# Optimization experiments

Hardware: AMD Instinct MI355X
Metric: run time of the kernel (lower is better)

## Reference

```python
import jax, jax.numpy as jnp
import numpy as np

N_NODES = 100000
N_EDGES = 3200000
IN_DIM = 256
HID = 64
OUT_DIM = 1


def gcn_conv(x, W, b, src, dst, n):
    # PyG GCNConv: h = x @ W; add self loops; sym-normalize; aggregate; + b
    h = x @ W  # [N, F]
    # degrees include self loops (edge_weight = 1), computed on target nodes
    ones = jnp.ones(src.shape[0], dtype=x.dtype)
    deg = jax.ops.segment_sum(ones, dst, num_segments=n) + 1.0  # +1 for self loop
    dinv = jax.lax.rsqrt(deg)
    norm = dinv[src] * dinv[dst]  # [E]
    msg = h[src] * norm[:, None]  # gather + scale
    out = jax.ops.segment_sum(msg, dst, num_segments=n)
    # self-loop contribution: norm_ii = dinv[i]^2
    out = out + h * (dinv * dinv)[:, None]
    return out + b


def setup_inputs() -> dict:
    key = jax.random.key(0)
    ks = jax.random.split(key, 6)
    x = jax.random.normal(ks[0], (N_NODES, IN_DIM), dtype=jnp.float32)
    edge_index = jax.random.randint(ks[1], (2, N_EDGES), 0, N_NODES, dtype=jnp.int64)
    W1 = jax.random.normal(ks[2], (IN_DIM, HID), dtype=jnp.float32) / np.sqrt(IN_DIM)
    b1 = jnp.zeros((HID,), dtype=jnp.float32)
    W2 = jax.random.normal(ks[3], (HID, HID), dtype=jnp.float32) / np.sqrt(HID)
    b2 = jnp.zeros((HID,), dtype=jnp.float32)
    Wf = jax.random.normal(ks[4], (HID, OUT_DIM), dtype=jnp.float32) / np.sqrt(HID)
    bf = jnp.zeros((OUT_DIM,), dtype=jnp.float32)
    return {"x": x, "edge_index": edge_index, "W1": W1, "b1": b1,
            "W2": W2, "b2": b2, "Wf": Wf, "bf": bf}


def reference(x, edge_index, W1, b1, W2, b2, Wf, bf):
    src, dst = edge_index[0], edge_index[1]
    n = x.shape[0]
    h = jax.nn.relu(gcn_conv(x, W1, b1, src, dst, n))
    h = jax.nn.relu(gcn_conv(h, W2, b2, src, dst, n))
    g = jnp.mean(h, axis=0)  # [HID] graph readout
    return jax.nn.sigmoid(g @ Wf + bf)  # [OUT_DIM]
```

## Files before the change

### kernel.cpp

```cpp
#include <hip/hip_runtime.h>


typedef unsigned int u32;
typedef unsigned short u16;
typedef unsigned char u8;
typedef short s16x8 __attribute__((ext_vector_type(8)));
typedef __bf16 bf16x8 __attribute__((ext_vector_type(8)));
typedef float f32x4 __attribute__((ext_vector_type(4)));

constexpr int HID  = 64;
constexpr int SH   = 7;
constexpr int BK   = 128;
constexpr int BPAD = 1024;
constexpr int CH   = 4096;
constexpr int SLOT = 5120;
constexpr int NBLK2 = 4096;

static __device__ __forceinline__ u8 f2fp8(float f) {
    int p = __builtin_amdgcn_cvt_pk_fp8_f32(f, f, 0, false);
    return (u8)(p & 0xFF);
}
static __device__ __forceinline__ float fp82f(u8 v) {
    return __builtin_amdgcn_cvt_f32_fp8((int)v, 0);
}
static __device__ __forceinline__ u16 f2bf(float f) {
    u32 u = __float_as_uint(f);
    return (u16)((u + 0x7FFFu + ((u >> 16) & 1u)) >> 16);
}

__global__ void pack_both_kernel(const float* __restrict__ W1, const float* __restrict__ W2,
                                 u16* __restrict__ wpack1, u16* __restrict__ wpack2) {
    int i = blockIdx.x * 256 + threadIdx.x;
    if (i < 256 * 64) {
        int e = i & 7, lane = (i >> 3) & 63, nt = (i >> 9) & 3, kk = i >> 11;
        wpack1[i] = f2bf(W1[(kk * 32 + (lane >> 4) * 8 + e) * HID + nt * 16 + (lane & 15)]);
    } else {
        int j = i - 256 * 64;
        if (j < 64 * 64) {
            int e = j & 7, lane = (j >> 3) & 63, nt = (j >> 9) & 3, kk = j >> 11;
            wpack2[j] = f2bf(W2[(kk * 32 + (lane >> 4) * 8 + e) * HID + nt * 16 + (lane & 15)]);
        }
    }
}

__global__ __launch_bounds__(256) void mega1_kernel(const int* __restrict__ src,
                                                    const int* __restrict__ dst,
                                                    int* __restrict__ bcur,
                                                    u32* __restrict__ ep, int ne,
                                                    const float* __restrict__ x,
                                                    const u16* __restrict__ wpack1,
                                                    u8* __restrict__ hp, int n,
                                                    int PBLK, int GBLK) {
    __shared__ int hcnt[BPAD];
    __shared__ int hoff[BPAD];
    __shared__ int gbase[BPAD];
    __shared__ u32 stage[CH];
    __shared__ int ssc[256];
    const int t = threadIdx.x;

    if ((int)blockIdx.x < PBLK) {
        const int base = blockIdx.x * CH;
        const int cnt = min(CH, ne - base);
        for (int i = t; i < BPAD; i += 256) hcnt[i] = 0;
        __syncthreads();
        int myr[CH / 256];
        #pragma unroll
        for (int k = 0; k < CH / 256; ++k) {
            int i = t + k * 256;
            if (i < cnt) myr[k] = atomicAdd(&hcnt[dst[base + i] >> SH], 1);
        }
        __syncthreads();
        {
            int c0 = hcnt[t*4], c1 = hcnt[t*4+1], c2 = hcnt[t*4+2], c3 = hcnt[t*4+3];
            int tsum = c0 + c1 + c2 + c3;
            ssc[t] = tsum; __syncthreads();
            int run = tsum;
            for (int off = 1; off < 256; off <<= 1) {
                int v = (t >= off) ? ssc[t - off] : 0;
                __syncthreads();
                run += v; ssc[t] = run;
                __syncthreads();
            }
            int ex = run - tsum;
            hoff[t*4] = ex; ex += c0;
            hoff[t*4+1] = ex; ex += c1;
            hoff[t*4+2] = ex; ex += c2;
            hoff[t*4+3] = ex;
        }
        __syncthreads();
        for (int b = t; b < BPAD; b += 256) {
            int c = hcnt[b];
            if (c) gbase[b] = b * SLOT + atomicAdd(&bcur[b], c);
        }
        #pragma unroll
        for (int k = 0; k < CH / 256; ++k) {
            int i = t + k * 256;
            if (i < cnt) {
                int s = src[base + i], d = dst[base + i];
                stage[hoff[d >> SH] + myr[k]] = ((u32)(d & (BK - 1)) << 20) | (u32)s;
            }
        }
        __syncthreads();
        for (int i = t; i < cnt; i += 256) {
            u32 v = stage[i];
            int lo = 0;
            #pragma unroll
            for (int s = 512; s; s >>= 1) {
                int m = lo + s;
                if (m < BPAD && hoff[m] <= i) lo = m;
            }
            ep[gbase[lo] + (i - hoff[lo])] = v;
        }
    } else {
        const int gbid = blockIdx.x - PBLK;
        const int lane = t & 63;
        const int wid = t >> 6;
        const int r16 = lane & 15;
        const int kgrp = lane >> 4;
        const int ntiles = (n + 15) >> 4;
        for (int tile = gbid * 4 + wid; tile < ntiles; tile += GBLK * 4) {
            const int row0 = tile * 16;
            const int arow = row0 + r16;
            f32x4 acc[4] = {f32x4{0,0,0,0}, f32x4{0,0,0,0}, f32x4{0,0,0,0}, f32x4{0,0,0,0}};
            #pragma unroll
            for (int kk = 0; kk < 256 / 32; ++kk) {
                s16x8 abits;
                if (arow < n) {
                    const float4* p0 = (const float4*)(x + (size_t)arow * 256 + kk * 32 + kgrp * 8);
                    float4 v0 = p0[0], v1 = p0[1];
                    abits[0] = (short)f2bf(v0.x); abits[1] = (short)f2bf(v0.y);
                    abits[2] = (short)f2bf(v0.z); abits[3] = (short)f2bf(v0.w);
                    abits[4] = (short)f2bf(v1.x); abits[5] = (short)f2bf(v1.y);
                    abits[6] = (short)f2bf(v1.z); abits[7] = (short)f2bf(v1.w);
                } else {
                    #pragma unroll
                    for (int j = 0; j < 8; ++j) abits[j] = 0;
                }
                bf16x8 afrag = __builtin_bit_cast(bf16x8, abits);
                const u16* wp = wpack1 + ((size_t)(kk * 4) * 64 + lane) * 8;
                #pragma unroll
                for (int nt = 0; nt < 4; ++nt) {
                    bf16x8 bfrag = *(const bf16x8*)(wp + (size_t)nt * 64 * 8);
                    acc[nt] = __builtin_amdgcn_mfma_f32_16x16x32_bf16(afrag, bfrag, acc[nt], 0, 0, 0);
                }
            }
            #pragma unroll
            for (int reg = 0; reg < 4; ++reg) {
                int r = row0 + kgrp * 4 + reg;
                if (r < n) {
                    #pragma unroll
                    for (int nt = 0; nt < 4; ++nt)
                        hp[(size_t)r * HID + nt * 16 + r16] = f2fp8(acc[nt][reg]);
                }
            }
        }
    }
}

__global__ __launch_bounds__(256) void bucket_sort_kernel(const u32* __restrict__ ep,
                                                          const int* __restrict__ bcur,
                                                          int* __restrict__ eidx,
                                                          int* __restrict__ rowend,
                                                          float* __restrict__ dinv,
                                                          u8* __restrict__ hp, int n) {
    __shared__ int cnt[BK];
    __shared__ int sc[BK];
    __shared__ int cur[BK];
    __shared__ float sdv[BK];
    const int t = threadIdx.x, b = blockIdx.x;
    const int beg = b * SLOT, end = b * SLOT + bcur[b];
    if (t < BK) cnt[t] = 0;
    __syncthreads();
    for (int p = beg + t; p < end; p += 256) atomicAdd(&cnt[ep[p] >> 20], 1);
    __syncthreads();
    if (t < BK) sc[t] = cnt[t];
    __syncthreads();
    for (int o = 1; o < BK; o <<= 1) {
        int v = 0;
        if (t < BK && t >= o) v = sc[t - o];
        __syncthreads();
        if (t < BK) sc[t] += v;
        __syncthreads();
    }
    if (t < BK) {
        int node = b * BK + t;
        float dv = rsqrtf((float)cnt[t] + 1.0f);
        sdv[t] = dv;
        if (node < n) {
            rowend[node] = beg + sc[t];
            dinv[node] = dv;
        }
        cur[t] = beg + sc[t] - cnt[t];
    }
    __syncthreads();
    for (int p = beg + t; p < end; p += 256) {
        u32 v = ep[p];
        int r = atomicAdd(&cur[v >> 20], 1);
        eidx[r] = (int)(v & 0xFFFFFu);
    }
    u32* hp32 = (u32*)hp;
    const int base_node = b * BK;
    for (int i = t; i < BK * 16; i += 256) {
        int r = i >> 4;
        int node = base_node + r;
        if (node < n) {
            size_t off = (size_t)node * 16 + (i & 15);
            u32 v = hp32[off];
            float dv = sdv[r];
            float f0 = __builtin_amdgcn_cvt_f32_fp8((int)v, 0) * dv;
            float f1 = __builtin_amdgcn_cvt_f32_fp8((int)v, 1) * dv;
            float f2 = __builtin_amdgcn_cvt_f32_fp8((int)v, 2) * dv;
            float f3 = __builtin_amdgcn_cvt_f32_fp8((int)v, 3) * dv;
            int pk = __builtin_amdgcn_cvt_pk_fp8_f32(f0, f1, 0, false);
            pk = __builtin_amdgcn_cvt_pk_fp8_f32(f2, f3, pk, true);
            hp32[off] = (u32)pk;
        }
    }
}

__global__ __launch_bounds__(256) void mfma_gemm2_kernel(const u8* __restrict__ A,
                                                         const u16* __restrict__ wpack,
                                                         const float* __restrict__ dinv,
                                                         u8* __restrict__ out8, int n) {
    const int t = threadIdx.x;
    const int lane = t & 63;
    const int wid = t >> 6;
    const int r16 = lane & 15;
    const int kgrp = lane >> 4;
    const int ntiles = (n + 15) >> 4;
    for (int tile = blockIdx.x * 4 + wid; tile < ntiles; tile += gridDim.x * 4) {
        const int row0 = tile * 16;
        const int arow = row0 + r16;
        f32x4 acc[4] = {f32x4{0,0,0,0}, f32x4{0,0,0,0}, f32x4{0,0,0,0}, f32x4{0,0,0,0}};
        #pragma unroll
        for (int kk = 0; kk < 2; ++kk) {
            s16x8 abits;
            u32 w0 = 0, w1 = 0;
            if (arow < n) {
                const u32* p0 = (const u32*)(A + (size_t)arow * 64 + kk * 32 + kgrp * 8);
                w0 = p0[0]; w1 = p0[1];
            }
            abits[0] = (short)f2bf(__builtin_amdgcn_cvt_f32_fp8((int)w0, 0));
            abits[1] = (short)f2bf(__builtin_amdgcn_cvt_f32_fp8((int)w0, 1));
            abits[2] = (short)f2bf(__builtin_amdgcn_cvt_f32_fp8((int)w0, 2));
            abits[3] = (short)f2bf(__builtin_amdgcn_cvt_f32_fp8((int)w0, 3));
            abits[4] = (short)f2bf(__builtin_amdgcn_cvt_f32_fp8((int)w1, 0));
            abits[5] = (short)f2bf(__builtin_amdgcn_cvt_f32_fp8((int)w1, 1));
            abits[6] = (short)f2bf(__builtin_amdgcn_cvt_f32_fp8((int)w1, 2));
            abits[7] = (short)f2bf(__builtin_amdgcn_cvt_f32_fp8((int)w1, 3));
            bf16x8 afrag = __builtin_bit_cast(bf16x8, abits);
            const u16* wp = wpack + ((size_t)(kk * 4) * 64 + lane) * 8;
            #pragma unroll
            for (int nt = 0; nt < 4; ++nt) {
                bf16x8 bfrag = *(const bf16x8*)(wp + (size_t)nt * 64 * 8);
                acc[nt] = __builtin_amdgcn_mfma_f32_16x16x32_bf16(afrag, bfrag, acc[nt], 0, 0, 0);
            }
        }
        #pragma unroll
        for (int reg = 0; reg < 4; ++reg) {
            int r = row0 + kgrp * 4 + reg;
            if (r < n) {
                float dv = dinv[r];
                #pragma unroll
                for (int nt = 0; nt < 4; ++nt)
                    out8[(size_t)r * HID + nt * 16 + r16] = f2fp8(acc[nt][reg] * dv);
            }
        }
    }
}

#define CVT4(acc0, acc1, acc2, acc3, wv) \
    acc0 += __builtin_amdgcn_cvt_f32_fp8((int)(wv), 0); \
    acc1 += __builtin_amdgcn_cvt_f32_fp8((int)(wv), 1); \
    acc2 += __builtin_amdgcn_cvt_f32_fp8((int)(wv), 2); \
    acc3 += __builtin_amdgcn_cvt_f32_fp8((int)(wv), 3);

__global__ __launch_bounds__(256) void agg_csr_kernel(const u8* __restrict__ hp,
                                                      const int* __restrict__ eidx,
                                                      const int* __restrict__ rowend,
                                                      const float* __restrict__ dinv,
                                                      const float* __restrict__ bias,
                                                      u8* __restrict__ out, int n) {
    int w = (blockIdx.x * 256 + threadIdx.x) >> 6;
    int lane = threadIdx.x & 63;
    if (w >= n) return;
    const int g = lane >> 4, fb = lane & 15;
    int beg = (w & (BK - 1)) ? rowend[w - 1] : (w >> SH) * SLOT;
    int end = rowend[w];
    float a0 = 0.f, a1 = 0.f, a2 = 0.f, a3 = 0.f;
    int p = beg;
    for (; p + 16 <= end; p += 16) {
        int s0 = __builtin_nontemporal_load(eidx + p + g);
        int s1 = __builtin_nontemporal_load(eidx + p + 4 + g);
        int s2 = __builtin_nontemporal_load(eidx + p + 8 + g);
        int s3 = __builtin_nontemporal_load(eidx + p + 12 + g);
        u32 w0 = *(const u32*)(hp + (size_t)s0 * 64 + fb * 4);
        u32 w1 = *(const u32*)(hp + (size_t)s1 * 64 + fb * 4);
        u32 w2 = *(const u32*)(hp + (size_t)s2 * 64 + fb * 4);
        u32 w3 = *(const u32*)(hp + (size_t)s3 * 64 + fb * 4);
        CVT4(a0, a1, a2, a3, w0)
        CVT4(a0, a1, a2, a3, w1)
        CVT4(a0, a1, a2, a3, w2)
        CVT4(a0, a1, a2, a3, w3)
    }
    for (; p < end; p += 4) {
        int idx = p + g;
        bool valid = idx < end;
        int s = __builtin_nontemporal_load(eidx + (valid ? idx : beg));
        u32 wv = *(const u32*)(hp + (size_t)s * 64 + fb * 4);
        if (valid) { CVT4(a0, a1, a2, a3, wv) }
    }
    a0 += __shfl_xor(a0, 16); a0 += __shfl_xor(a0, 32);
    a1 += __shfl_xor(a1, 16); a1 += __shfl_xor(a1, 32);
    a2 += __shfl_xor(a2, 16); a2 += __shfl_xor(a2, 32);
    a3 += __shfl_xor(a3, 16); a3 += __shfl_xor(a3, 32);
    u32 sv = *(const u32*)(hp + (size_t)w * 64 + fb * 4);
    float dv = dinv[w];
    float v0 = fmaxf(dv * (a0 + __builtin_amdgcn_cvt_f32_fp8((int)sv, 0)) + bias[fb * 4 + 0], 0.f);
    float v1 = fmaxf(dv * (a1 + __builtin_amdgcn_cvt_f32_fp8((int)sv, 1)) + bias[fb * 4 + 1], 0.f);
    float v2 = fmaxf(dv * (a2 + __builtin_amdgcn_cvt_f32_fp8((int)sv, 2)) + bias[fb * 4 + 2], 0.f);
    float v3 = fmaxf(dv * (a3 + __builtin_amdgcn_cvt_f32_fp8((int)sv, 3)) + bias[fb * 4 + 3], 0.f);
    if (g == 0) {
        int r = __builtin_amdgcn_cvt_pk_fp8_f32(v0, v1, 0, false);
        r = __builtin_amdgcn_cvt_pk_fp8_f32(v2, v3, r, true);
        *(u32*)(out + (size_t)w * 64 + fb * 4) = (u32)r;
    }
}

__global__ __launch_bounds__(256) void agg_csr_reduce_kernel(const u8* __restrict__ hp,
                                                             const int* __restrict__ eidx,
                                                             const int* __restrict__ rowend,
                                                             const float* __restrict__ dinv,
                                                             const float* __restrict__ bias,
                                                             float* __restrict__ partials, int n) {
    __shared__ float sred[256];
    int t = threadIdx.x, lane = t & 63;
    const int g = lane >> 4, fb = lane & 15;
    int wid = (blockIdx.x * 256 + t) >> 6;
    int wstride = gridDim.x * 4;
    float bl0 = bias[fb * 4 + 0], bl1 = bias[fb * 4 + 1];
    float bl2 = bias[fb * 4 + 2], bl3 = bias[fb * 4 + 3];
    float t0 = 0.f, t1 = 0.f, t2 = 0.f, t3 = 0.f;
    for (int w = wid; w < n; w += wstride) {
        int beg = (w & (BK - 1)) ? rowend[w - 1] : (w >> SH) * SLOT;
        int end = rowend[w];
        float a0 = 0.f, a1 = 0.f, a2 = 0.f, a3 = 0.f;
        int p = beg;
        for (; p + 16 <= end; p += 16) {
            int s0 = __builtin_nontemporal_load(eidx + p + g);
            int s1 = __builtin_nontemporal_load(eidx + p + 4 + g);
            int s2 = __builtin_nontemporal_load(eidx + p + 8 + g);
            int s3 = __builtin_nontemporal_load(eidx + p + 12 + g);
            u32 w0 = *(const u32*)(hp + (size_t)s0 * 64 + fb * 4);
            u32 w1 = *(const u32*)(hp + (size_t)s1 * 64 + fb * 4);
            u32 w2 = *(const u32*)(hp + (size_t)s2 * 64 + fb * 4);
            u32 w3 = *(const u32*)(hp + (size_t)s3 * 64 + fb * 4);
            CVT4(a0, a1, a2, a3, w0)
            CVT4(a0, a1, a2, a3, w1)
            CVT4(a0, a1, a2, a3, w2)
            CVT4(a0, a1, a2, a3, w3)
        }
        for (; p < end; p += 4) {
            int idx = p + g;
            bool valid = idx < end;
            int s = __builtin_nontemporal_load(eidx + (valid ? idx : beg));
            u32 wv = *(const u32*)(hp + (size_t)s * 64 + fb * 4);
            if (valid) { CVT4(a0, a1, a2, a3, wv) }
        }
        a0 += __shfl_xor(a0, 16); a0 += __shfl_xor(a0, 32);
        a1 += __shfl_xor(a1, 16); a1 += __shfl_xor(a1, 32);
        a2 += __shfl_xor(a2, 16); a2 += __shfl_xor(a2, 32);
        a3 += __shfl_xor(a3, 16); a3 += __shfl_xor(a3, 32);
        u32 sv = *(const u32*)(hp + (size_t)w * 64 + fb * 4);
        float dv = dinv[w];
        t0 += fmaxf(dv * (a0 + __builtin_amdgcn_cvt_f32_fp8((int)sv, 0)) + bl0, 0.f);
        t1 += fmaxf(dv * (a1 + __builtin_amdgcn_cvt_f32_fp8((int)sv, 1)) + bl1, 0.f);
        t2 += fmaxf(dv * (a2 + __builtin_amdgcn_cvt_f32_fp8((int)sv, 2)) + bl2, 0.f);
        t3 += fmaxf(dv * (a3 + __builtin_amdgcn_cvt_f32_fp8((int)sv, 3)) + bl3, 0.f);
    }
    int wv_ = t >> 6;
    if (g == 0) {
        sred[wv_ * 64 + fb * 4 + 0] = t0;
        sred[wv_ * 64 + fb * 4 + 1] = t1;
        sred[wv_ * 64 + fb * 4 + 2] = t2;
        sred[wv_ * 64 + fb * 4 + 3] = t3;
    }
    __syncthreads();
    if (t < 64) partials[blockIdx.x * 64 + t] = sred[t] + sred[t + 64] + sred[t + 128] + sred[t + 192];
}

__global__ __launch_bounds__(256) void gsum_stage_kernel(const float* __restrict__ parts, int nblk,
                                                         float* __restrict__ gsum) {
    __shared__ float sred[256];
    int t = threadIdx.x, col = t & 63;
    float a = 0.f;
    for (int bk = blockIdx.x * 4 + (t >> 6); bk < nblk; bk += gridDim.x * 4)
        a += parts[bk * 64 + col];
    sred[t] = a; __syncthreads();
    if (t < 64) atomicAdd(&gsum[t], sred[t] + sred[t + 64] + sred[t + 128] + sred[t + 192]);
}

__global__ void final_gsum_kernel(const float* __restrict__ gsum, const float* __restrict__ Wf,
                                  const float* __restrict__ bf_, float* __restrict__ out, float invn) {
    int lane = threadIdx.x;
    float v = gsum[lane] * invn * Wf[lane];
    #pragma unroll
    for (int off = 32; off; off >>= 1) v += __shfl_down(v, off);
    if (lane == 0) out[0] = 1.f / (1.f + expf(-(v + bf_[0])));
}

template <int K, typename TIn>
__global__ __launch_bounds__(256) void gemm_scale_kernel(const TIn* __restrict__ A,
                                                         const float* __restrict__ W,
                                                         const float* __restrict__ dinv,
                                                         u8* __restrict__ out8, int n) {
    __shared__ float xs[16][K];
    const int t = threadIdx.x;
    const int row0 = blockIdx.x * 16;
    if constexpr (sizeof(TIn) == 4) {
        const float* Af = (const float*)A;
        for (int i = t; i < 16 * K; i += 256) {
            int r = i / K;
            (&xs[0][0])[i] = (row0 + r < n) ? Af[(size_t)row0 * K + i] : 0.f;
        }
    } else {
        const u8* Ab = (const u8*)A;
        for (int i = t; i < 16 * K; i += 256) {
            int r = i / K;
            (&xs[0][0])[i] = (row0 + r < n) ? fp82f(Ab[(size_t)row0 * K + i]) : 0.f;
        }
    }
    __syncthreads();
    const int c = t & 63, rg = t >> 6;
    float acc[4] = {0.f, 0.f, 0.f, 0.f};
    #pragma unroll 4
    for (int k = 0; k < K; ++k) {
        float w = W[k * HID + c];
        #pragma unroll
        for (int j = 0; j < 4; ++j) acc[j] += xs[rg + 4 * j][k] * w;
    }
    #pragma unroll
    for (int j = 0; j < 4; ++j) {
        int r = row0 + rg + 4 * j;
        if (r < n) out8[(size_t)r * HID + c] = f2fp8(acc[j] * dinv[r]);
    }
}
__global__ void deg_f_kernel(const int* __restrict__ dst, float* __restrict__ deg, int ne) {
    int i = blockIdx.x * blockDim.x + threadIdx.x, st = gridDim.x * blockDim.x;
    for (; i < ne; i += st) atomicAdd(&deg[dst[i]], 1.0f);
}
__global__ void dinvf_kernel(float* __restrict__ deg, int n) {
    int i = blockIdx.x * blockDim.x + threadIdx.x;
    if (i < n) deg[i] = rsqrtf(deg[i] + 1.0f);
}
__global__ __launch_bounds__(256) void aggregate_atomic_kernel(const u8* __restrict__ hp,
        const int* __restrict__ src, const int* __restrict__ dst,
        const float* __restrict__ dinv, float* __restrict__ outf, int ne) {
    size_t tt = (size_t)blockIdx.x * 256 + threadIdx.x;
    int e = (int)(tt >> 6), f = (int)(tt & 63);
    if (e >= ne) return;
    int s = src[e], d = dst[e];
    atomicAdd(&outf[(size_t)d * HID + f], fp82f(hp[s * HID + f]) * dinv[d]);
}
__global__ void finalize1_fb_kernel(u8* __restrict__ hp, const float* __restrict__ agg,
                                    const float* __restrict__ dinv, const float* __restrict__ b, int n) {
    size_t i = (size_t)blockIdx.x * blockDim.x + threadIdx.x;
    if (i >= (size_t)n * HID) return;
    int node = (int)(i >> 6);
    float v = agg[i] + fp82f(hp[i]) * dinv[node] + b[i & 63];
    hp[i] = f2fp8(fmaxf(v, 0.f));
}
__global__ __launch_bounds__(256) void finalize2_fb_kernel(const u8* __restrict__ hp,
        const float* __restrict__ agg, const float* __restrict__ dinv,
        const float* __restrict__ b, float* __restrict__ gsum, int n) {
    __shared__ float sred[256];
    const int t = threadIdx.x, c = t & 63;
    const size_t total = (size_t)n * HID;
    const size_t stride = (size_t)gridDim.x * blockDim.x;
    float acc = 0.f;
    for (size_t i = (size_t)blockIdx.x * blockDim.x + t; i < total; i += stride) {
        int node = (int)(i >> 6);
        acc += fmaxf(agg[i] + fp82f(hp[i]) * dinv[node] + b[c], 0.f);
    }
    sred[t] = acc; __syncthreads();
    if (t < 64) atomicAdd(&gsum[c], sred[t] + sred[t + 64] + sred[t + 128] + sred[t + 192]);
}
__global__ void final_gsum_fb_kernel(const float* __restrict__ gsum, const float* __restrict__ Wf,
                                     const float* __restrict__ bf_, float* __restrict__ out, int n) {
    int lane = threadIdx.x;
    float v = (gsum[lane] / (float)n) * Wf[lane];
    #pragma unroll
    for (int off = 32; off; off >>= 1) v += __shfl_down(v, off);
    if (lane == 0) out[0] = 1.f / (1.f + expf(-(v + bf_[0])));
}

extern "C" void kernel_launch(void* const* d_in, const int* in_sizes, int n_in,
                              void* d_out, int out_size, void* d_ws, size_t ws_size,
                              hipStream_t stream) {
    const float* x  = (const float*)d_in[0];
    const int*   ei = (const int*)d_in[1];
    const float* W1 = (const float*)d_in[2];
    const float* b1 = (const float*)d_in[3];
    const float* W2 = (const float*)d_in[4];
    const float* b2 = (const float*)d_in[5];
    const float* Wf = (const float*)d_in[6];
    const float* bf_ = (const float*)d_in[7];
    float* out = (float*)d_out;

    const int n  = in_sizes[0] / 256;
    const int ne = in_sizes[1] / 2;
    const int* srcp = ei;
    const int* dstp = ei + ne;
    const int B = (n + BK - 1) / BK;

    char* p = (char*)d_ws;
    u32*   ep     = (u32*)p;   p += ((size_t)B * SLOT + 4096) * 4;
    int*   bcur   = (int*)p;   p += BPAD * 4;
    float* gsum   = (float*)p; p += 64 * 4;
    float* dinv   = (float*)p; p += (size_t)n * 4;
    int*   rowend = (int*)p;   p += (size_t)n * 4;
    int*   eidx   = (int*)p;   p += ((size_t)B * SLOT + 4096) * 4;
    float* parts  = (float*)p; p += (size_t)NBLK2 * 64 * 4;
    p = (char*)(((uintptr_t)p + 15) & ~(uintptr_t)15);
    u16*   wpack1 = (u16*)p;   p += 256 * 64 * 2;
    u16*   wpack2 = (u16*)p;   p += 64 * 64 * 2;
    u8*    hp     = (u8*)p;    p += (size_t)n * HID;
    u8*    h1     = (u8*)p;    p += (size_t)n * HID;
    size_t need = (size_t)(p - (char*)d_ws);

    bool slack_ok = ((size_t)ne / (size_t)B) <= (size_t)(SLOT - 1024);

    if (ws_size >= need && n <= (1 << 17) && slack_ok) {
        (void)hipMemsetAsync(bcur, 0, (BPAD + 64) * 4, stream);
        pack_both_kernel<<<80, 256, 0, stream>>>(W1, W2, wpack1, wpack2);

        const int PBLK = (ne + CH - 1) / CH;
        const int ntiles = (n + 15) / 16;
        const int GBLK = (ntiles + 3) / 4;
        mega1_kernel<<<PBLK + GBLK, 256, 0, stream>>>(srcp, dstp, bcur, ep, ne,
                                                      x, wpack1, hp, n, PBLK, GBLK);
        bucket_sort_kernel<<<B, 256, 0, stream>>>(ep, bcur, eidx, rowend, dinv, hp, n);
        agg_csr_kernel<<<(n + 3) / 4, 256, 0, stream>>>(hp, eidx, rowend, dinv, b1, h1, n);
        mfma_gemm2_kernel<<<GBLK, 256, 0, stream>>>(h1, wpack2, dinv, hp, n);
        agg_csr_reduce_kernel<<<NBLK2, 256, 0, stream>>>(hp, eidx, rowend, dinv, b2, parts, n);
        gsum_stage_kernel<<<128, 256, 0, stream>>>(parts, NBLK2, gsum);
        final_gsum_kernel<<<1, 64, 0, stream>>>(gsum, Wf, bf_, out, 1.0f / (float)n);
    } else {
        char* q = (char*)d_ws;
        float* dinvF = (float*)q; q += (size_t)n * 4;
        float* gsumF = (float*)q; q += 64 * 4;
        u8*    hpF   = (u8*)q;   q += (size_t)n * HID;
        float* aggF  = (float*)q;

        (void)hipMemsetAsync(dinvF, 0, ((size_t)n + 64) * 4, stream);
        deg_f_kernel<<<2048, 256, 0, stream>>>(dstp, dinvF, ne);
        dinvf_kernel<<<(n + 255) / 256, 256, 0, stream>>>(dinvF, n);

        gemm_scale_kernel<256, float><<<(n + 15) / 16, 256, 0, stream>>>(x, W1, dinvF, hpF, n);
        (void)hipMemsetAsync(aggF, 0, (size_t)n * HID * 4, stream);
        aggregate_atomic_kernel<<<(int)(((size_t)ne * 64 + 255) / 256), 256, 0, stream>>>(hpF, srcp, dstp, dinvF, aggF, ne);
        finalize1_fb_kernel<<<(int)(((size_t)n * HID + 255) / 256), 256, 0, stream>>>(hpF, aggF, dinvF, b1, n);

        gemm_scale_kernel<64, u8><<<(n + 15) / 16, 256, 0, stream>>>(hpF, W2, dinvF, hpF, n);
        (void)hipMemsetAsync(aggF, 0, (size_t)n * HID * 4, stream);
        aggregate_atomic_kernel<<<(int)(((size_t)ne * 64 + 255) / 256), 256, 0, stream>>>(hpF, srcp, dstp, dinvF, aggF, ne);
        finalize2_fb_kernel<<<2048, 256, 0, stream>>>(hpF, aggF, dinvF, b2, gsumF, n);
        final_gsum_fb_kernel<<<1, 64, 0, stream>>>(gsumF, Wf, bf_, out, n);
    }
}
```

Before: 248.7 us.

## Move layer-1 GEMM from partition kernel into per-bucket sort kernel

```diff
diff --git a/kernel.cpp b/kernel.cpp
--- a/kernel.cpp
+++ b/kernel.cpp
@@ -43,126 +43,79 @@
     }
 }
 
-__global__ __launch_bounds__(256) void mega1_kernel(const int* __restrict__ src,
-                                                    const int* __restrict__ dst,
-                                                    int* __restrict__ bcur,
-                                                    u32* __restrict__ ep, int ne,
-                                                    const float* __restrict__ x,
-                                                    const u16* __restrict__ wpack1,
-                                                    u8* __restrict__ hp, int n,
-                                                    int PBLK, int GBLK) {
+__global__ __launch_bounds__(256) void partition_kernel(const int* __restrict__ src,
+                                                        const int* __restrict__ dst,
+                                                        int* __restrict__ bcur,
+                                                        u32* __restrict__ ep, int ne) {
     __shared__ int hcnt[BPAD];
     __shared__ int hoff[BPAD];
     __shared__ int gbase[BPAD];
     __shared__ u32 stage[CH];
     __shared__ int ssc[256];
     const int t = threadIdx.x;
-
-    if ((int)blockIdx.x < PBLK) {
-        const int base = blockIdx.x * CH;
-        const int cnt = min(CH, ne - base);
-        for (int i = t; i < BPAD; i += 256) hcnt[i] = 0;
-        __syncthreads();
-        int myr[CH / 256];
+    const int base = blockIdx.x * CH;
+    const int cnt = min(CH, ne - base);
+    for (int i = t; i < BPAD; i += 256) hcnt[i] = 0;
+    __syncthreads();
+
+    int myr[CH / 256];
+    #pragma unroll
+    for (int k = 0; k < CH / 256; ++k) {
+        int i = t + k * 256;
+        if (i < cnt) myr[k] = atomicAdd(&hcnt[dst[base + i] >> SH], 1);
+    }
+    __syncthreads();
+    {
+        int c0 = hcnt[t*4], c1 = hcnt[t*4+1], c2 = hcnt[t*4+2], c3 = hcnt[t*4+3];
+        int tsum = c0 + c1 + c2 + c3;
+        ssc[t] = tsum; __syncthreads();
+        int run = tsum;
+        for (int off = 1; off < 256; off <<= 1) {
+            int v = (t >= off) ? ssc[t - off] : 0;
+            __syncthreads();
+            run += v; ssc[t] = run;
+            __syncthreads();
+        }
+        int ex = run - tsum;
+        hoff[t*4] = ex; ex += c0;
+        hoff[t*4+1] = ex; ex += c1;
+        hoff[t*4+2] = ex; ex += c2;
+        hoff[t*4+3] = ex;
+    }
+    __syncthreads();
+    for (int b = t; b < BPAD; b += 256) {
+        int c = hcnt[b];
+        if (c) gbase[b] = b * SLOT + atomicAdd(&bcur[b], c);
+    }
+    #pragma unroll
+    for (int k = 0; k < CH / 256; ++k) {
+        int i = t + k * 256;
+        if (i < cnt) {
+            int s = src[base + i], d = dst[base + i];
+            stage[hoff[d >> SH] + myr[k]] = ((u32)(d & (BK - 1)) << 20) | (u32)s;
+        }
+    }
+    __syncthreads();
+    for (int i = t; i < cnt; i += 256) {
+        u32 v = stage[i];
+        int lo = 0;
         #pragma unroll
-        for (int k = 0; k < CH / 256; ++k) {
-            int i = t + k * 256;
-            if (i < cnt) myr[k] = atomicAdd(&hcnt[dst[base + i] >> SH], 1);
-        }
-        __syncthreads();
-        {
-            int c0 = hcnt[t*4], c1 = hcnt[t*4+1], c2 = hcnt[t*4+2], c3 = hcnt[t*4+3];
-            int tsum = c0 + c1 + c2 + c3;
-            ssc[t] = tsum; __syncthreads();
-            int run = tsum;
-            for (int off = 1; off < 256; off <<= 1) {
-                int v = (t >= off) ? ssc[t - off] : 0;
-                __syncthreads();
-                run += v; ssc[t] = run;
-                __syncthreads();
-            }
-            int ex = run - tsum;
-            hoff[t*4] = ex; ex += c0;
-            hoff[t*4+1] = ex; ex += c1;
-            hoff[t*4+2] = ex; ex += c2;
-            hoff[t*4+3] = ex;
-        }
-        __syncthreads();
-        for (int b = t; b < BPAD; b += 256) {
-            int c = hcnt[b];
-            if (c) gbase[b] = b * SLOT + atomicAdd(&bcur[b], c);
-        }
-        #pragma unroll
-        for (int k = 0; k < CH / 256; ++k) {
-            int i = t + k * 256;
-            if (i < cnt) {
-                int s = src[base + i], d = dst[base + i];
-                stage[hoff[d >> SH] + myr[k]] = ((u32)(d & (BK - 1)) << 20) | (u32)s;
-            }
-        }
-        __syncthreads();
-        for (int i = t; i < cnt; i += 256) {
-            u32 v = stage[i];
-            int lo = 0;
-            #pragma unroll
-            for (int s = 512; s; s >>= 1) {
-                int m = lo + s;
-                if (m < BPAD && hoff[m] <= i) lo = m;
-            }
-            ep[gbase[lo] + (i - hoff[lo])] = v;
-        }
-    } else {
-        const int gbid = blockIdx.x - PBLK;
-        const int lane = t & 63;
-        const int wid = t >> 6;
-        const int r16 = lane & 15;
-        const int kgrp = lane >> 4;
-        const int ntiles = (n + 15) >> 4;
-        for (int tile = gbid * 4 + wid; tile < ntiles; tile += GBLK * 4) {
-            const int row0 = tile * 16;
-            const int arow = row0 + r16;
-            f32x4 acc[4] = {f32x4{0,0,0,0}, f32x4{0,0,0,0}, f32x4{0,0,0,0}, f32x4{0,0,0,0}};
-            #pragma unroll
-            for (int kk = 0; kk < 256 / 32; ++kk) {
-                s16x8 abits;
-                if (arow < n) {
-                    const float4* p0 = (const float4*)(x + (size_t)arow * 256 + kk * 32 + kgrp * 8);
-                    float4 v0 = p0[0], v1 = p0[1];
-                    abits[0] = (short)f2bf(v0.x); abits[1] = (short)f2bf(v0.y);
-                    abits[2] = (short)f2bf(v0.z); abits[3] = (short)f2bf(v0.w);
-                    abits[4] = (short)f2bf(v1.x); abits[5] = (short)f2bf(v1.y);
-                    abits[6] = (short)f2bf(v1.z); abits[7] = (short)f2bf(v1.w);
-                } else {
-                    #pragma unroll
-                    for (int j = 0; j < 8; ++j) abits[j] = 0;
-                }
-                bf16x8 afrag = __builtin_bit_cast(bf16x8, abits);
-                const u16* wp = wpack1 + ((size_t)(kk * 4) * 64 + lane) * 8;
-                #pragma unroll
-                for (int nt = 0; nt < 4; ++nt) {
-                    bf16x8 bfrag = *(const bf16x8*)(wp + (size_t)nt * 64 * 8);
-                    acc[nt] = __builtin_amdgcn_mfma_f32_16x16x32_bf16(afrag, bfrag, acc[nt], 0, 0, 0);
-                }
-            }
-            #pragma unroll
-            for (int reg = 0; reg < 4; ++reg) {
-                int r = row0 + kgrp * 4 + reg;
-                if (r < n) {
-                    #pragma unroll
-                    for (int nt = 0; nt < 4; ++nt)
-                        hp[(size_t)r * HID + nt * 16 + r16] = f2fp8(acc[nt][reg]);
-                }
-            }
-        }
-    }
-}
-
-__global__ __launch_bounds__(256) void bucket_sort_kernel(const u32* __restrict__ ep,
-                                                          const int* __restrict__ bcur,
-                                                          int* __restrict__ eidx,
-                                                          int* __restrict__ rowend,
-                                                          float* __restrict__ dinv,
-                                                          u8* __restrict__ hp, int n) {
+        for (int s = 512; s; s >>= 1) {
+            int m = lo + s;
+            if (m < BPAD && hoff[m] <= i) lo = m;
+        }
+        ep[gbase[lo] + (i - hoff[lo])] = v;
+    }
+}
+
+__global__ __launch_bounds__(256) void sortgemm_kernel(const u32* __restrict__ ep,
+                                                       const int* __restrict__ bcur,
+                                                       int* __restrict__ eidx,
+                                                       int* __restrict__ rowend,
+                                                       float* __restrict__ dinv,
+                                                       const float* __restrict__ x,
+                                                       const u16* __restrict__ wpack1,
+                                                       u8* __restrict__ hp, int n) {
     __shared__ int cnt[BK];
     __shared__ int sc[BK];
     __shared__ int cur[BK];
@@ -198,22 +151,49 @@
         int r = atomicAdd(&cur[v >> 20], 1);
         eidx[r] = (int)(v & 0xFFFFFu);
     }
-    u32* hp32 = (u32*)hp;
-    const int base_node = b * BK;
-    for (int i = t; i < BK * 16; i += 256) {
-        int r = i >> 4;
-        int node = base_node + r;
-        if (node < n) {
-            size_t off = (size_t)node * 16 + (i & 15);
-            u32 v = hp32[off];
-            float dv = sdv[r];
-            float f0 = __builtin_amdgcn_cvt_f32_fp8((int)v, 0) * dv;
-            float f1 = __builtin_amdgcn_cvt_f32_fp8((int)v, 1) * dv;
-            float f2 = __builtin_amdgcn_cvt_f32_fp8((int)v, 2) * dv;
-            float f3 = __builtin_amdgcn_cvt_f32_fp8((int)v, 3) * dv;
-            int pk = __builtin_amdgcn_cvt_pk_fp8_f32(f0, f1, 0, false);
-            pk = __builtin_amdgcn_cvt_pk_fp8_f32(f2, f3, pk, true);
-            hp32[off] = (u32)pk;
+    __syncthreads();
+
+    const int lane = t & 63;
+    const int wid = t >> 6;
+    const int r16 = lane & 15;
+    const int kgrp = lane >> 4;
+    #pragma unroll
+    for (int it = 0; it < 2; ++it) {
+        const int lrow0 = (wid * 2 + it) * 16;
+        const int row0 = b * BK + lrow0;
+        const int arow = row0 + r16;
+        f32x4 acc[4] = {f32x4{0,0,0,0}, f32x4{0,0,0,0}, f32x4{0,0,0,0}, f32x4{0,0,0,0}};
+        #pragma unroll
+        for (int kk = 0; kk < 8; ++kk) {
+            s16x8 abits;
+            if (arow < n) {
+                const float4* p0 = (const float4*)(x + (size_t)arow * 256 + kk * 32 + kgrp * 8);
+                float4 v0 = p0[0], v1 = p0[1];
+                abits[0] = (short)f2bf(v0.x); abits[1] = (short)f2bf(v0.y);
+                abits[2] = (short)f2bf(v0.z); abits[3] = (short)f2bf(v0.w);
+                abits[4] = (short)f2bf(v1.x); abits[5] = (short)f2bf(v1.y);
+                abits[6] = (short)f2bf(v1.z); abits[7] = (short)f2bf(v1.w);
+            } else {
+                #pragma unroll
+                for (int j = 0; j < 8; ++j) abits[j] = 0;
+            }
+            bf16x8 afrag = __builtin_bit_cast(bf16x8, abits);
+            const u16* wp = wpack1 + ((size_t)(kk * 4) * 64 + lane) * 8;
+            #pragma unroll
+            for (int nt = 0; nt < 4; ++nt) {
+                bf16x8 bfrag = *(const bf16x8*)(wp + (size_t)nt * 64 * 8);
+                acc[nt] = __builtin_amdgcn_mfma_f32_16x16x32_bf16(afrag, bfrag, acc[nt], 0, 0, 0);
+            }
+        }
+        #pragma unroll
+        for (int reg = 0; reg < 4; ++reg) {
+            int r = row0 + kgrp * 4 + reg;
+            if (r < n) {
+                float dv = sdv[lrow0 + kgrp * 4 + reg];
+                #pragma unroll
+                for (int nt = 0; nt < 4; ++nt)
+                    hp[(size_t)r * HID + nt * 16 + r16] = f2fp8(acc[nt][reg] * dv);
+            }
         }
     }
 }
@@ -537,9 +517,8 @@
         const int PBLK = (ne + CH - 1) / CH;
         const int ntiles = (n + 15) / 16;
         const int GBLK = (ntiles + 3) / 4;
-        mega1_kernel<<<PBLK + GBLK, 256, 0, stream>>>(srcp, dstp, bcur, ep, ne,
-                                                      x, wpack1, hp, n, PBLK, GBLK);
-        bucket_sort_kernel<<<B, 256, 0, stream>>>(ep, bcur, eidx, rowend, dinv, hp, n);
+        partition_kernel<<<PBLK, 256, 0, stream>>>(srcp, dstp, bcur, ep, ne);
+        sortgemm_kernel<<<B, 256, 0, stream>>>(ep, bcur, eidx, rowend, dinv, x, wpack1, hp, n);
         agg_csr_kernel<<<(n + 3) / 4, 256, 0, stream>>>(hp, eidx, rowend, dinv, b1, h1, n);
         mfma_gemm2_kernel<<<GBLK, 256, 0, stream>>>(h1, wpack2, dinv, hp, n);
         agg_csr_reduce_kernel<<<NBLK2, 256, 0, stream>>>(hp, eidx, rowend, dinv, b2, parts, n);
```

Result: no change. 253.0 us (+1.7%).
